# Kernel optimization log

Hardware: AMD Instinct MI355X
Metric: run time of the kernel (lower is better)

The kernel has to match this reference:

```python
import jax, jax.numpy as jnp
import numpy as np

N = 100000   # nodes
E = 1600000  # edges (avg degree 16)
F_IN, H1, H2, H3, C = 500, 200, 100, 40, 3


def setup_inputs() -> dict:
    key = jax.random.key(0)
    ks = jax.random.split(key, 10)
    def w(k, shape, fan_in):
        return jax.random.normal(k, shape, dtype=jnp.float32) / np.sqrt(fan_in)
    return {
        "x": jax.random.normal(ks[0], (N, F_IN), dtype=jnp.float32),
        "edge_index": jax.random.randint(ks[1], (2, E), 0, N, dtype=jnp.int32),
        "W1": w(ks[2], (H1, F_IN), F_IN), "b1": jnp.zeros((H1,), jnp.float32),
        "W1b": w(ks[3], (H2, H1), H1),  "b1b": jnp.zeros((H2,), jnp.float32),
        "W2b": w(ks[4], (H3, H2), H2),  "b2b": jnp.zeros((H3,), jnp.float32),
        "W2": w(ks[5], (C, H3), H3),    "b2": jnp.zeros((C,), jnp.float32),
    }


def _gcn_conv(x, W, b, src, dst, norm_e, n):
    # GCNConv: linear transform, then normalized scatter-add aggregation, then bias
    h = x @ W.T                                   # [N, out]
    msgs = h[src] * norm_e[:, None]               # [E+N, out] gathered, normalized
    out = jax.ops.segment_sum(msgs, dst, num_segments=n)
    return out + b


def reference(x, edge_index, W1, b1, W1b, b1b, W2b, b2b, W2, b2):
    n = x.shape[0]
    loop = jnp.arange(n, dtype=edge_index.dtype)
    src = jnp.concatenate([edge_index[0], loop])  # add self-loops (GCNConv default)
    dst = jnp.concatenate([edge_index[1], loop])
    # symmetric normalization: deg computed on target nodes, norm = d^-1/2[src]*d^-1/2[dst]
    deg = jax.ops.segment_sum(jnp.ones_like(dst, dtype=x.dtype), dst, num_segments=n)
    dinv = jnp.where(deg > 0, jax.lax.rsqrt(deg), 0.0)
    norm_e = dinv[src] * dinv[dst]

    # dropout(p=0.5, training=self.training) is identity at inference
    h = jax.nn.relu(_gcn_conv(x, W1, b1, src, dst, norm_e, n))
    h = jax.nn.relu(_gcn_conv(h, W1b, b1b, src, dst, norm_e, n))
    h = jax.nn.relu(_gcn_conv(h, W2b, b2b, src, dst, norm_e, n))
    return _gcn_conv(h, W2, b2, src, dst, norm_e, n)
```

## Files before the change

### kernel.cpp

```cpp
#include <hip/hip_runtime.h>


#define DEV __device__ __forceinline__

typedef __attribute__((ext_vector_type(8))) short short8;
typedef __attribute__((ext_vector_type(8))) _Float16 f16x8;
typedef __attribute__((ext_vector_type(4))) float f32x4;
typedef __attribute__((ext_vector_type(4))) _Float16 f16x4;

DEV unsigned short f2bf(float x) {
    unsigned u = __builtin_bit_cast(unsigned, x);
    u += 0x7FFFu + ((u >> 16) & 1u);
    return (unsigned short)(u >> 16);
}
DEV float bf2f(unsigned short b) {
    return __builtin_bit_cast(float, (unsigned)b << 16);
}

DEV void gload_lds16(const void* g, void* l) {
    __builtin_amdgcn_global_load_lds(
        (const __attribute__((address_space(1))) unsigned int*)g,
        (__attribute__((address_space(3))) unsigned int*)l, 16, 0, 0);
}


__global__ void k_init(int* __restrict__ cnt, int* __restrict__ fill, int n) {
    int i = blockIdx.x * 256 + threadIdx.x;
    if (i < n) { cnt[i] = 1; fill[i] = 0; }
}

__global__ void k_count(const int* __restrict__ dst, int* __restrict__ cnt, int E) {
    int e = blockIdx.x * 256 + threadIdx.x;
    if (e < E) atomicAdd(&cnt[dst[e]], 1);
}

__global__ void k_scan1(const int* __restrict__ cnt, int* __restrict__ row_start,
                        int* __restrict__ partial, float* __restrict__ dinv, int n) {
    __shared__ int sdata[256];
    int base = blockIdx.x * 1024;
    int t = threadIdx.x;
    int v[4]; int sum = 0;
#pragma unroll
    for (int j = 0; j < 4; ++j) {
        int idx = base + t * 4 + j;
        v[j] = (idx < n) ? cnt[idx] : 0;
        if (idx < n) dinv[idx] = rsqrtf((float)v[j]);
        sum += v[j];
    }
    sdata[t] = sum;
    __syncthreads();
    for (int off = 1; off < 256; off <<= 1) {
        int x = (t >= off) ? sdata[t - off] : 0;
        __syncthreads();
        sdata[t] += x;
        __syncthreads();
    }
    int excl = sdata[t] - sum;
#pragma unroll
    for (int j = 0; j < 4; ++j) {
        int idx = base + t * 4 + j;
        if (idx < n) row_start[idx] = excl;
        excl += v[j];
    }
    if (t == 255) partial[blockIdx.x] = sdata[255];
}

__global__ void k_scan2(int* __restrict__ partial, int nb) {
    __shared__ int s[128];
    int t = threadIdx.x;
    int v = (t < nb) ? partial[t] : 0;
    s[t] = v;
    __syncthreads();
    for (int off = 1; off < 128; off <<= 1) {
        int x = (t >= off) ? s[t - off] : 0;
        __syncthreads();
        s[t] += x;
        __syncthreads();
    }
    if (t < nb) partial[t] = s[t] - v;
}

__global__ void k_scan3(int* __restrict__ row_start, const int* __restrict__ partial,
                        int n, int total) {
    int i = blockIdx.x * 256 + threadIdx.x;
    if (i < n) row_start[i] += partial[i >> 10];
    if (i == 0) row_start[n] = total;
}

__global__ void k_fill(const int* __restrict__ src, const int* __restrict__ dst,
                       const int* __restrict__ row_start, int* __restrict__ fill,
                       int* __restrict__ csr_src, int E, int n) {
    int i = blockIdx.x * 256 + threadIdx.x;
    int total = E + n;
    if (i >= total) return;
    int s, d;
    if (i < E) { s = src[i]; d = dst[i]; }
    else       { s = d = i - E; }
    int pos = row_start[d] + atomicAdd(&fill[d], 1);
    csr_src[pos] = s;
}

__global__ void k_wdec(const float* __restrict__ W, int N, int K,
                       unsigned short* __restrict__ Wh, unsigned short* __restrict__ Wl,
                       int NPAD, int KPAD) {
    int i = blockIdx.x * 256 + threadIdx.x;
    if (i >= NPAD * KPAD) return;
    int r = i / KPAD, k = i - r * KPAD;
    float x = (r < N && k < K) ? W[r * K + k] : 0.f;
    unsigned short h = f2bf(x);
    unsigned short l = f2bf(x - bf2f(h));
    Wh[i] = h; Wl[i] = l;
}
__global__ void k_wdec16(const float* __restrict__ W, int N, int K,
                         unsigned short* __restrict__ Wh, unsigned short* __restrict__ Wl,
                         int NPAD, int KPAD) {
    int i = blockIdx.x * 256 + threadIdx.x;
    if (i >= NPAD * KPAD) return;
    int r = i / KPAD, k = i - r * KPAD;
    float x = (r < N && k < K) ? W[r * K + k] : 0.f;
    _Float16 h = (_Float16)x;
    _Float16 l = (_Float16)((x - (float)h) * 2048.0f);
    Wh[i] = __builtin_bit_cast(unsigned short, h);
    Wl[i] = __builtin_bit_cast(unsigned short, l);
}


struct A8 { f32x4 lo, hi; };

template <int NF, int MODE, typename AT>
__global__ __launch_bounds__(256, 2)
void gemm_mfma(const AT* __restrict__ A, int lda, int M, int K,
               const unsigned short* __restrict__ Wh,
               const unsigned short* __restrict__ Wl, int ldw,
               const float* __restrict__ dinv,
               _Float16* __restrict__ H16, int ldh, int Nout) {
    constexpr int NPAD = NF * 16;
    constexpr int HBUF = NPAD * 64;
    constexpr int BUFB = 2 * HBUF;
    constexpr int CH   = NPAD * 4;
    constexpr int CH2  = 2 * CH;
    constexpr int NISS = CH2 / 64;
    __shared__ char lds[2 * BUFB];

    const int tid  = threadIdx.x;
    const int wv   = tid >> 6;
    const int lane = tid & 63;
    const int lr   = lane & 15;
    const int kq   = lane >> 4;
    const int m0   = blockIdx.x * 128;

    int arow0 = m0 + wv * 32 + lr;       if (arow0 >= M) arow0 = M - 1;
    int arow1 = m0 + wv * 32 + 16 + lr;  if (arow1 >= M) arow1 = M - 1;
    const AT* Arow0 = A + (size_t)arow0 * lda;
    const AT* Arow1 = A + (size_t)arow1 * lda;

    auto stageW = [&](int s, int bufsel) {
        const int kb = s * 32;
        char* base = lds + bufsel * BUFB;
        for (int i = wv; i < NISS; i += 4) {
            int c  = i * 64 + lane;
            int h  = (c >= CH) ? 1 : 0;
            int cc = c - h * CH;
            int r  = cc >> 2;
            int sl = cc & 3;
            int gs = sl ^ (r & 3);
            const unsigned short* gp = (h ? Wl : Wh) + (size_t)r * ldw + kb + gs * 8;
            gload_lds16(gp, base + i * 1024);
        }
    };

    auto loadA32 = [&](const AT* Arow, int s) -> A8 {
        A8 o;
        int kb = s * 32 + kq * 8;
        if (kb + 8 <= K) {
            const float* ap = (const float*)Arow + kb;
            o.lo = *(const f32x4*)ap;
            o.hi = *(const f32x4*)(ap + 4);
        } else {
#pragma unroll
            for (int i = 0; i < 4; ++i) {
                int k0 = kb + i, k1 = kb + 4 + i;
                o.lo[i] = (k0 < K) ? (float)Arow[k0] : 0.f;
                o.hi[i] = (k1 < K) ? (float)Arow[k1] : 0.f;
            }
        }
        return o;
    };
    auto loadA16 = [&](const AT* Arow, int s) -> short8 {
        int kb = s * 32 + kq * 8;
        if (kb + 8 <= K) return *(const short8*)((const unsigned short*)Arow + kb);
        short8 o;
        const unsigned short* ap = (const unsigned short*)Arow;
#pragma unroll
        for (int i = 0; i < 8; ++i) o[i] = (kb + i < K) ? (short)ap[kb + i] : (short)0;
        return o;
    };

    f32x4 acP[NF], acQ[NF], alP[NF], alQ[NF];
#pragma unroll
    for (int f = 0; f < NF; ++f) {
        acP[f] = (f32x4){0.f, 0.f, 0.f, 0.f};
        acQ[f] = (f32x4){0.f, 0.f, 0.f, 0.f};
        alP[f] = (f32x4){0.f, 0.f, 0.f, 0.f};
        alQ[f] = (f32x4){0.f, 0.f, 0.f, 0.f};
    }

    const int nsteps = ldw / 32;

    stageW(0, 0);
    A8 a0c{}, a1c{}; short8 h0c{}, h1c{};
    if constexpr (MODE == 0) { a0c = loadA32(Arow0, 0); a1c = loadA32(Arow1, 0); }
    else                     { h0c = loadA16(Arow0, 0); h1c = loadA16(Arow1, 0); }
    __syncthreads();

    const int ro = lr * 64 + ((kq ^ (lr & 3)) << 4);

    for (int s = 0; s < nsteps; ++s) {
        const char* bb = lds + (s & 1) * BUFB;
        const bool more = (s + 1 < nsteps);

        if (more) stageW(s + 1, (s + 1) & 1);
        A8 a0n{}, a1n{}; short8 h0n{}, h1n{};
        if (more) {
            if constexpr (MODE == 0) { a0n = loadA32(Arow0, s + 1); a1n = loadA32(Arow1, s + 1); }
            else                     { h0n = loadA16(Arow0, s + 1); h1n = loadA16(Arow1, s + 1); }
        }

        if constexpr (MODE == 0) {
            float av0[8], av1[8];
#pragma unroll
            for (int i = 0; i < 4; ++i) {
                av0[i] = a0c.lo[i]; av0[4 + i] = a0c.hi[i];
                av1[i] = a1c.lo[i]; av1[4 + i] = a1c.hi[i];
            }
            short8 a0hi, a0lo, a1hi, a1lo;
#pragma unroll
            for (int i = 0; i < 8; ++i) {
                unsigned short h0 = f2bf(av0[i]);
                a0hi[i] = (short)h0; a0lo[i] = (short)f2bf(av0[i] - bf2f(h0));
                unsigned short h1 = f2bf(av1[i]);
                a1hi[i] = (short)h1; a1lo[i] = (short)f2bf(av1[i] - bf2f(h1));
            }
#pragma unroll
            for (int f = 0; f < NF; ++f) {
                short8 bh = *(const short8*)(bb + f * 1024 + ro);
                short8 bl = *(const short8*)(bb + HBUF + f * 1024 + ro);
                acP[f] = __builtin_amdgcn_mfma_f32_16x16x32_bf16(a0hi, bh, acP[f], 0, 0, 0);
                acP[f] = __builtin_amdgcn_mfma_f32_16x16x32_bf16(a0hi, bl, acP[f], 0, 0, 0);
                acP[f] = __builtin_amdgcn_mfma_f32_16x16x32_bf16(a0lo, bh, acP[f], 0, 0, 0);
                acQ[f] = __builtin_amdgcn_mfma_f32_16x16x32_bf16(a1hi, bh, acQ[f], 0, 0, 0);
                acQ[f] = __builtin_amdgcn_mfma_f32_16x16x32_bf16(a1hi, bl, acQ[f], 0, 0, 0);
                acQ[f] = __builtin_amdgcn_mfma_f32_16x16x32_bf16(a1lo, bh, acQ[f], 0, 0, 0);
            }
        } else {
            f16x8 a0 = __builtin_bit_cast(f16x8, h0c);
            f16x8 a1 = __builtin_bit_cast(f16x8, h1c);
#pragma unroll
            for (int f = 0; f < NF; ++f) {
                f16x8 bh = __builtin_bit_cast(f16x8, *(const short8*)(bb + f * 1024 + ro));
                f16x8 bl = __builtin_bit_cast(f16x8, *(const short8*)(bb + HBUF + f * 1024 + ro));
                acP[f] = __builtin_amdgcn_mfma_f32_16x16x32_f16(a0, bh, acP[f], 0, 0, 0);
                alP[f] = __builtin_amdgcn_mfma_f32_16x16x32_f16(a0, bl, alP[f], 0, 0, 0);
                acQ[f] = __builtin_amdgcn_mfma_f32_16x16x32_f16(a1, bh, acQ[f], 0, 0, 0);
                alQ[f] = __builtin_amdgcn_mfma_f32_16x16x32_f16(a1, bl, alQ[f], 0, 0, 0);
            }
        }

        __syncthreads();
        if constexpr (MODE == 0) { a0c = a0n; a1c = a1n; }
        else                     { h0c = h0n; h1c = h1n; }
    }

    {
        const int rbase = m0 + wv * 32 + kq * 4;
        float dv[4];
#pragma unroll
        for (int j = 0; j < 4; ++j) {
            int row = rbase + j;
            dv[j] = (row < M) ? dinv[row] : 0.f;
        }
#pragma unroll
        for (int f = 0; f < NF; ++f) {
            int col = f * 16 + lr;
            if (col >= Nout) continue;
#pragma unroll
            for (int j = 0; j < 4; ++j) {
                int row = rbase + j;
                if (row >= M) continue;
                float v = acP[f][j];
                if constexpr (MODE == 1) v += alP[f][j] * (1.0f / 2048.0f);
                H16[(size_t)row * ldh + col] = (_Float16)(v * dv[j]);
            }
        }
    }
    {
        const int rbase = m0 + wv * 32 + 16 + kq * 4;
        float dv[4];
#pragma unroll
        for (int j = 0; j < 4; ++j) {
            int row = rbase + j;
            dv[j] = (row < M) ? dinv[row] : 0.f;
        }
#pragma unroll
        for (int f = 0; f < NF; ++f) {
            int col = f * 16 + lr;
            if (col >= Nout) continue;
#pragma unroll
            for (int j = 0; j < 4; ++j) {
                int row = rbase + j;
                if (row >= M) continue;
                float v = acQ[f][j];
                if constexpr (MODE == 1) v += alQ[f][j] * (1.0f / 2048.0f);
                H16[(size_t)row * ldh + col] = (_Float16)(v * dv[j]);
            }
        }
    }
}


template <int F, bool RELU>
__global__ __launch_bounds__(256)
void agg_f16(const _Float16* __restrict__ h, const int* __restrict__ row_start,
             const int* __restrict__ csr_src, const float* __restrict__ dinv,
             const float* __restrict__ bias, _Float16* __restrict__ out, int n,
             int ldo) {
    constexpr int LPN = F / 4;
    constexpr int NPW = 64 / LPN;
    int wave = blockIdx.x * 4 + (threadIdx.x >> 6);
    int lane = threadIdx.x & 63;
    int sub  = lane / LPN;
    int fi   = lane - sub * LPN;
    int node = wave * NPW + sub;
    if (sub >= NPW || node >= n) return;
    int f = fi * 4;
    const _Float16* hf = h + f;

    f32x4 acc = {0.f, 0.f, 0.f, 0.f};
    int e0 = row_start[node], e1 = row_start[node + 1];
    int e = e0;
    for (; e + 4 <= e1; e += 4) {
        int s0 = csr_src[e + 0];
        int s1 = csr_src[e + 1];
        int s2 = csr_src[e + 2];
        int s3 = csr_src[e + 3];
        f16x4 v0 = *(const f16x4*)&hf[(size_t)s0 * F];
        f16x4 v1 = *(const f16x4*)&hf[(size_t)s1 * F];
        f16x4 v2 = *(const f16x4*)&hf[(size_t)s2 * F];
        f16x4 v3 = *(const f16x4*)&hf[(size_t)s3 * F];
        acc += __builtin_convertvector(v0, f32x4);
        acc += __builtin_convertvector(v1, f32x4);
        acc += __builtin_convertvector(v2, f32x4);
        acc += __builtin_convertvector(v3, f32x4);
    }
    for (; e < e1; ++e) {
        int s = csr_src[e];
        f16x4 v = *(const f16x4*)&hf[(size_t)s * F];
        acc += __builtin_convertvector(v, f32x4);
    }
    float dn = dinv[node];
    f32x4 b4 = *(const f32x4*)&bias[f];
    acc = acc * dn + b4;
    if (RELU) {
#pragma unroll
        for (int j = 0; j < 4; ++j) acc[j] = fmaxf(acc[j], 0.f);
    }
    f16x4 o;
#pragma unroll
    for (int j = 0; j < 4; ++j) o[j] = (_Float16)acc[j];
    *(f16x4*)&out[(size_t)node * ldo + f] = o;
}


__global__ void gemm_small(const _Float16* __restrict__ A, const float* __restrict__ B,
                           const float* __restrict__ dinv, float* __restrict__ C,
                           int M, int K) {
    int m = blockIdx.x * 256 + threadIdx.x;
    if (m >= M) return;
    float a0 = 0.f, a1 = 0.f, a2 = 0.f;
    for (int k = 0; k < K; ++k) {
        float a = (float)A[(size_t)m * K + k];
        a0 += a * B[0 * K + k];
        a1 += a * B[1 * K + k];
        a2 += a * B[2 * K + k];
    }
    float dv = dinv[m];
    C[(size_t)m * 3 + 0] = a0 * dv;
    C[(size_t)m * 3 + 1] = a1 * dv;
    C[(size_t)m * 3 + 2] = a2 * dv;
}

__global__ void agg_f3(const float* __restrict__ h, const int* __restrict__ row_start,
                       const int* __restrict__ csr_src, const float* __restrict__ dinv,
                       const float* __restrict__ bias, float* __restrict__ out, int n) {
    int i = blockIdx.x * 256 + threadIdx.x;
    if (i >= n * 3) return;
    int node = i / 3;
    int f = i - node * 3;
    float acc = 0.f;
    int e1 = row_start[node + 1];
    for (int e = row_start[node]; e < e1; ++e) {
        int s = csr_src[e];
        acc += h[(size_t)s * 3 + f];
    }
    out[i] = acc * dinv[node] + bias[f];
}


extern "C" void kernel_launch(void* const* d_in, const int* in_sizes, int n_in,
                              void* d_out, int out_size, void* d_ws, size_t ws_size,
                              hipStream_t stream) {
    const float* x   = (const float*)d_in[0];
    const int*   ei  = (const int*)d_in[1];
    const float* W1  = (const float*)d_in[2];
    const float* b1  = (const float*)d_in[3];
    const float* W1b = (const float*)d_in[4];
    const float* b1b = (const float*)d_in[5];
    const float* W2b = (const float*)d_in[6];
    const float* b2b = (const float*)d_in[7];
    const float* W2  = (const float*)d_in[8];
    const float* b2  = (const float*)d_in[9];
    float* out = (float*)d_out;

    const int F_IN = 500, H1 = 200, H2 = 100, H3 = 40;
    const int N = in_sizes[0] / F_IN;
    const int E = in_sizes[1] / 2;
    const int* src = ei;
    const int* dst = ei + E;

    size_t off = 0;
    auto alloc = [&](size_t bytes) -> void* {
        void* p = (char*)d_ws + off;
        off += (bytes + 255) & ~(size_t)255;
        return p;
    };
    int*   cnt       = (int*)  alloc((size_t)N * 4);
    int*   row_start = (int*)  alloc((size_t)(N + 1) * 4);
    int*   fill      = (int*)  alloc((size_t)N * 4);
    int*   partial   = (int*)  alloc(128 * 4);
    float* dinv      = (float*)alloc((size_t)N * 4);
    int*   csr_src   = (int*)  alloc((size_t)(E + N) * 4);
    unsigned short* wh1 = (unsigned short*)alloc(208 * 512 * 2);
    unsigned short* wl1 = (unsigned short*)alloc(208 * 512 * 2);
    unsigned short* wh2 = (unsigned short*)alloc(112 * 224 * 2);
    unsigned short* wl2 = (unsigned short*)alloc(112 * 224 * 2);
    unsigned short* wh3 = (unsigned short*)alloc(48 * 128 * 2);
    unsigned short* wl3 = (unsigned short*)alloc(48 * 128 * 2);
    _Float16* h16   = (_Float16*)alloc((size_t)N * H1 * 2);
    _Float16* act16 = (_Float16*)alloc((size_t)N * H1 * 2);
    float*    bufC  = (float*)   alloc((size_t)N * 3 * 4);

    int gN  = (N + 255) / 256;
    int gE  = (E + 255) / 256;
    int gEN = (E + N + 255) / 256;
    int nb  = (N + 1023) / 1024;

    k_init <<<gN, 256, 0, stream>>>(cnt, fill, N);
    k_count<<<gE, 256, 0, stream>>>(dst, cnt, E);
    k_scan1<<<nb, 256, 0, stream>>>(cnt, row_start, partial, dinv, N);
    k_scan2<<<1, 128, 0, stream>>>(partial, nb);
    k_scan3<<<gN, 256, 0, stream>>>(row_start, partial, N, E + N);
    k_fill <<<gEN, 256, 0, stream>>>(src, dst, row_start, fill, csr_src, E, N);

    k_wdec  <<<(208 * 512 + 255) / 256, 256, 0, stream>>>(W1,  H1, F_IN, wh1, wl1, 208, 512);
    k_wdec16<<<(112 * 224 + 255) / 256, 256, 0, stream>>>(W1b, H2, H1,   wh2, wl2, 112, 224);
    k_wdec16<<<( 48 * 128 + 255) / 256, 256, 0, stream>>>(W2b, H3, H2,   wh3, wl3,  48, 128);

    const int gG = (N + 127) / 128;

    gemm_mfma<13, 0, float><<<gG, 256, 0, stream>>>(x, F_IN, N, F_IN, wh1, wl1, 512,
                                                    dinv, h16, H1, H1);
    agg_f16<200, true><<<(N + 3) / 4, 256, 0, stream>>>(h16, row_start, csr_src, dinv,
                                                        b1, act16, N, 200);
    gemm_mfma<7, 1, _Float16><<<gG, 256, 0, stream>>>(act16, 200, N, H1, wh2, wl2, 224,
                                                      dinv, h16, H2, H2);
    agg_f16<100, true><<<(N / 2 + 3) / 4, 256, 0, stream>>>(h16, row_start, csr_src, dinv,
                                                            b1b, act16, N, 112);
    gemm_mfma<3, 1, _Float16><<<gG, 256, 0, stream>>>(act16, 112, N, H2, wh3, wl3, 128,
                                                      dinv, h16, H3, H3);
    {
        int waves = (N + 5) / 6, blocks = (waves + 3) / 4;
        agg_f16<40, true><<<blocks, 256, 0, stream>>>(h16, row_start, csr_src, dinv,
                                                      b2b, act16, N, 40);
    }
    gemm_small<<<(N + 255) / 256, 256, 0, stream>>>(act16, W2, dinv, bufC, N, H3);
    agg_f3<<<(N * 3 + 255) / 256, 256, 0, stream>>>(bufC, row_start, csr_src, dinv,
                                                    b2, out, N);
}
```

Measured before the change: 577.3 us.

## Load GEMM weights directly from global memory instead of LDS double-buffering

Removes the LDS staging of weight tiles, the double buffer and the per-step barriers from the MFMA GEMM. Each lane now reads its weight fragments straight from global memory, relying on L1/L2 caching of the small weight matrices. Blocks grow to 512 threads covering 256 rows, and the K dimension becomes a compile-time template parameter. The A-operand prefetch is also dropped, so load latency is exposed unless occupancy hides it, and weight reads are now redundant across waves.

```diff
diff --git a/kernel.cpp b/kernel.cpp
--- a/kernel.cpp
+++ b/kernel.cpp
@@ -15,12 +15,6 @@
 }
 DEV float bf2f(unsigned short b) {
     return __builtin_bit_cast(float, (unsigned)b << 16);
-}
-
-DEV void gload_lds16(const void* g, void* l) {
-    __builtin_amdgcn_global_load_lds(
-        (const __attribute__((address_space(1))) unsigned int*)g,
-        (__attribute__((address_space(3))) unsigned int*)l, 16, 0, 0);
 }
 
 
@@ -127,47 +121,27 @@
 
 struct A8 { f32x4 lo, hi; };
 
-template <int NF, int MODE, typename AT>
-__global__ __launch_bounds__(256, 2)
+template <int NF, int LDW, int MODE, typename AT>
+__global__ __launch_bounds__(512, 2)
 void gemm_mfma(const AT* __restrict__ A, int lda, int M, int K,
                const unsigned short* __restrict__ Wh,
-               const unsigned short* __restrict__ Wl, int ldw,
+               const unsigned short* __restrict__ Wl,
                const float* __restrict__ dinv,
                _Float16* __restrict__ H16, int ldh, int Nout) {
-    constexpr int NPAD = NF * 16;
-    constexpr int HBUF = NPAD * 64;
-    constexpr int BUFB = 2 * HBUF;
-    constexpr int CH   = NPAD * 4;
-    constexpr int CH2  = 2 * CH;
-    constexpr int NISS = CH2 / 64;
-    __shared__ char lds[2 * BUFB];
-
     const int tid  = threadIdx.x;
     const int wv   = tid >> 6;
     const int lane = tid & 63;
     const int lr   = lane & 15;
     const int kq   = lane >> 4;
-    const int m0   = blockIdx.x * 128;
+    const int m0   = blockIdx.x * 256;
 
     int arow0 = m0 + wv * 32 + lr;       if (arow0 >= M) arow0 = M - 1;
     int arow1 = m0 + wv * 32 + 16 + lr;  if (arow1 >= M) arow1 = M - 1;
     const AT* Arow0 = A + (size_t)arow0 * lda;
     const AT* Arow1 = A + (size_t)arow1 * lda;
 
-    auto stageW = [&](int s, int bufsel) {
-        const int kb = s * 32;
-        char* base = lds + bufsel * BUFB;
-        for (int i = wv; i < NISS; i += 4) {
-            int c  = i * 64 + lane;
-            int h  = (c >= CH) ? 1 : 0;
-            int cc = c - h * CH;
-            int r  = cc >> 2;
-            int sl = cc & 3;
-            int gs = sl ^ (r & 3);
-            const unsigned short* gp = (h ? Wl : Wh) + (size_t)r * ldw + kb + gs * 8;
-            gload_lds16(gp, base + i * 1024);
-        }
-    };
+    const unsigned short* WhL = Wh + (size_t)lr * LDW + kq * 8;
+    const unsigned short* WlL = Wl + (size_t)lr * LDW + kq * 8;
 
     auto loadA32 = [&](const AT* Arow, int s) -> A8 {
         A8 o;
@@ -205,33 +179,20 @@
         alQ[f] = (f32x4){0.f, 0.f, 0.f, 0.f};
     }
 
-    const int nsteps = ldw / 32;
-
-    stageW(0, 0);
-    A8 a0c{}, a1c{}; short8 h0c{}, h1c{};
-    if constexpr (MODE == 0) { a0c = loadA32(Arow0, 0); a1c = loadA32(Arow1, 0); }
-    else                     { h0c = loadA16(Arow0, 0); h1c = loadA16(Arow1, 0); }
-    __syncthreads();
-
-    const int ro = lr * 64 + ((kq ^ (lr & 3)) << 4);
+    constexpr int nsteps = LDW / 32;
 
     for (int s = 0; s < nsteps; ++s) {
-        const char* bb = lds + (s & 1) * BUFB;
-        const bool more = (s + 1 < nsteps);
-
-        if (more) stageW(s + 1, (s + 1) & 1);
-        A8 a0n{}, a1n{}; short8 h0n{}, h1n{};
-        if (more) {
-            if constexpr (MODE == 0) { a0n = loadA32(Arow0, s + 1); a1n = loadA32(Arow1, s + 1); }
-            else                     { h0n = loadA16(Arow0, s + 1); h1n = loadA16(Arow1, s + 1); }
-        }
+        const unsigned short* wph = WhL + s * 32;
+        const unsigned short* wpl = WlL + s * 32;
 
         if constexpr (MODE == 0) {
+            A8 a0 = loadA32(Arow0, s);
+            A8 a1 = loadA32(Arow1, s);
             float av0[8], av1[8];
 #pragma unroll
             for (int i = 0; i < 4; ++i) {
-                av0[i] = a0c.lo[i]; av0[4 + i] = a0c.hi[i];
-                av1[i] = a1c.lo[i]; av1[4 + i] = a1c.hi[i];
+                av0[i] = a0.lo[i]; av0[4 + i] = a0.hi[i];
+                av1[i] = a1.lo[i]; av1[4 + i] = a1.hi[i];
             }
             short8 a0hi, a0lo, a1hi, a1lo;
 #pragma unroll
@@ -243,8 +204,8 @@
             }
 #pragma unroll
             for (int f = 0; f < NF; ++f) {
-                short8 bh = *(const short8*)(bb + f * 1024 + ro);
-                short8 bl = *(const short8*)(bb + HBUF + f * 1024 + ro);
+                short8 bh = *(const short8*)(wph + (size_t)f * 16 * LDW);
+                short8 bl = *(const short8*)(wpl + (size_t)f * 16 * LDW);
                 acP[f] = __builtin_amdgcn_mfma_f32_16x16x32_bf16(a0hi, bh, acP[f], 0, 0, 0);
                 acP[f] = __builtin_amdgcn_mfma_f32_16x16x32_bf16(a0hi, bl, acP[f], 0, 0, 0);
                 acP[f] = __builtin_amdgcn_mfma_f32_16x16x32_bf16(a0lo, bh, acP[f], 0, 0, 0);
@@ -253,22 +214,18 @@
                 acQ[f] = __builtin_amdgcn_mfma_f32_16x16x32_bf16(a1lo, bh, acQ[f], 0, 0, 0);
             }
         } else {
-            f16x8 a0 = __builtin_bit_cast(f16x8, h0c);
-            f16x8 a1 = __builtin_bit_cast(f16x8, h1c);
+            f16x8 a0 = __builtin_bit_cast(f16x8, loadA16(Arow0, s));
+            f16x8 a1 = __builtin_bit_cast(f16x8, loadA16(Arow1, s));
 #pragma unroll
             for (int f = 0; f < NF; ++f) {
-                f16x8 bh = __builtin_bit_cast(f16x8, *(const short8*)(bb + f * 1024 + ro));
-                f16x8 bl = __builtin_bit_cast(f16x8, *(const short8*)(bb + HBUF + f * 1024 + ro));
+                f16x8 bh = __builtin_bit_cast(f16x8, *(const short8*)(wph + (size_t)f * 16 * LDW));
+                f16x8 bl = __builtin_bit_cast(f16x8, *(const short8*)(wpl + (size_t)f * 16 * LDW));
                 acP[f] = __builtin_amdgcn_mfma_f32_16x16x32_f16(a0, bh, acP[f], 0, 0, 0);
                 alP[f] = __builtin_amdgcn_mfma_f32_16x16x32_f16(a0, bl, alP[f], 0, 0, 0);
                 acQ[f] = __builtin_amdgcn_mfma_f32_16x16x32_f16(a1, bh, acQ[f], 0, 0, 0);
                 alQ[f] = __builtin_amdgcn_mfma_f32_16x16x32_f16(a1, bl, alQ[f], 0, 0, 0);
             }
         }
-
-        __syncthreads();
-        if constexpr (MODE == 0) { a0c = a0n; a1c = a1n; }
-        else                     { h0c = h0n; h1c = h1n; }
     }
 
     {
@@ -465,18 +422,18 @@
     k_wdec16<<<(112 * 224 + 255) / 256, 256, 0, stream>>>(W1b, H2, H1,   wh2, wl2, 112, 224);
     k_wdec16<<<( 48 * 128 + 255) / 256, 256, 0, stream>>>(W2b, H3, H2,   wh3, wl3,  48, 128);
 
-    const int gG = (N + 127) / 128;
-
-    gemm_mfma<13, 0, float><<<gG, 256, 0, stream>>>(x, F_IN, N, F_IN, wh1, wl1, 512,
-                                                    dinv, h16, H1, H1);
+    const int gG = (N + 255) / 256;
+
+    gemm_mfma<13, 512, 0, float><<<gG, 512, 0, stream>>>(x, F_IN, N, F_IN, wh1, wl1,
+                                                         dinv, h16, H1, H1);
     agg_f16<200, true><<<(N + 3) / 4, 256, 0, stream>>>(h16, row_start, csr_src, dinv,
                                                         b1, act16, N, 200);
-    gemm_mfma<7, 1, _Float16><<<gG, 256, 0, stream>>>(act16, 200, N, H1, wh2, wl2, 224,
-                                                      dinv, h16, H2, H2);
+    gemm_mfma<7, 224, 1, _Float16><<<gG, 512, 0, stream>>>(act16, 200, N, H1, wh2, wl2,
+                                                           dinv, h16, H2, H2);
     agg_f16<100, true><<<(N / 2 + 3) / 4, 256, 0, stream>>>(h16, row_start, csr_src, dinv,
                                                             b1b, act16, N, 112);
-    gemm_mfma<3, 1, _Float16><<<gG, 256, 0, stream>>>(act16, 112, N, H2, wh3, wl3, 128,
-                                                      dinv, h16, H3, H3);
+    gemm_mfma<3, 128, 1, _Float16><<<gG, 512, 0, stream>>>(act16, 112, N, H2, wh3, wl3,
+                                                           dinv, h16, H3, H3);
     {
         int waves = (N + 5) / 6, blocks = (waves + 3) / 4;
         agg_f16<40, true><<<blocks, 256, 0, stream>>>(h16, row_start, csr_src, dinv,
```

After: 780.9 us. +35.3%, slower.

## Use fp16 split-weight MFMA for first layer and split columns across 8 waves

Applied to the files above, without the earlier changes.

The first GEMM no longer splits x into bf16 hi/lo parts with three bf16 MFMAs per tile. It now converts x to a single fp16 value and uses the fp16 hi/lo weight split already used by the other layers, so all layers share one code path. Each GEMM block grows to 512 threads, with wave pairs splitting the output column fragments, which halves accumulator registers per wave and adds parallelism. The risk is accuracy: x is rounded to fp16 and its low part is dropped, and fp16 has less exponent range than bf16.

```diff
diff --git a/kernel.cpp b/kernel.cpp
--- a/kernel.cpp
+++ b/kernel.cpp
@@ -7,15 +7,6 @@
 typedef __attribute__((ext_vector_type(8))) _Float16 f16x8;
 typedef __attribute__((ext_vector_type(4))) float f32x4;
 typedef __attribute__((ext_vector_type(4))) _Float16 f16x4;
-
-DEV unsigned short f2bf(float x) {
-    unsigned u = __builtin_bit_cast(unsigned, x);
-    u += 0x7FFFu + ((u >> 16) & 1u);
-    return (unsigned short)(u >> 16);
-}
-DEV float bf2f(unsigned short b) {
-    return __builtin_bit_cast(float, (unsigned)b << 16);
-}
 
 DEV void gload_lds16(const void* g, void* l) {
     __builtin_amdgcn_global_load_lds(
@@ -100,17 +91,7 @@
     csr_src[pos] = s;
 }
 
-__global__ void k_wdec(const float* __restrict__ W, int N, int K,
-                       unsigned short* __restrict__ Wh, unsigned short* __restrict__ Wl,
-                       int NPAD, int KPAD) {
-    int i = blockIdx.x * 256 + threadIdx.x;
-    if (i >= NPAD * KPAD) return;
-    int r = i / KPAD, k = i - r * KPAD;
-    float x = (r < N && k < K) ? W[r * K + k] : 0.f;
-    unsigned short h = f2bf(x);
-    unsigned short l = f2bf(x - bf2f(h));
-    Wh[i] = h; Wl[i] = l;
-}
+
 __global__ void k_wdec16(const float* __restrict__ W, int N, int K,
                          unsigned short* __restrict__ Wh, unsigned short* __restrict__ Wl,
                          int NPAD, int KPAD) {
@@ -128,7 +109,7 @@
 struct A8 { f32x4 lo, hi; };
 
 template <int NF, int MODE, typename AT>
-__global__ __launch_bounds__(256, 2)
+__global__ __launch_bounds__(512, 2)
 void gemm_mfma(const AT* __restrict__ A, int lda, int M, int K,
                const unsigned short* __restrict__ Wh,
                const unsigned short* __restrict__ Wl, int ldw,
@@ -140,24 +121,28 @@
     constexpr int CH   = NPAD * 4;
     constexpr int CH2  = 2 * CH;
     constexpr int NISS = CH2 / 64;
+    constexpr int FC   = (NF + 1) / 2;
     __shared__ char lds[2 * BUFB];
 
     const int tid  = threadIdx.x;
     const int wv   = tid >> 6;
+    const int rg   = wv >> 1;
+    const int cg   = wv & 1;
     const int lane = tid & 63;
     const int lr   = lane & 15;
     const int kq   = lane >> 4;
     const int m0   = blockIdx.x * 128;
-
-    int arow0 = m0 + wv * 32 + lr;       if (arow0 >= M) arow0 = M - 1;
-    int arow1 = m0 + wv * 32 + 16 + lr;  if (arow1 >= M) arow1 = M - 1;
+    const int f0   = cg * FC;
+
+    int arow0 = m0 + rg * 32 + lr;       if (arow0 >= M) arow0 = M - 1;
+    int arow1 = m0 + rg * 32 + 16 + lr;  if (arow1 >= M) arow1 = M - 1;
     const AT* Arow0 = A + (size_t)arow0 * lda;
     const AT* Arow1 = A + (size_t)arow1 * lda;
 
     auto stageW = [&](int s, int bufsel) {
         const int kb = s * 32;
         char* base = lds + bufsel * BUFB;
-        for (int i = wv; i < NISS; i += 4) {
+        for (int i = wv; i < NISS; i += 8) {
             int c  = i * 64 + lane;
             int h  = (c >= CH) ? 1 : 0;
             int cc = c - h * CH;
@@ -195,14 +180,23 @@
         for (int i = 0; i < 8; ++i) o[i] = (kb + i < K) ? (short)ap[kb + i] : (short)0;
         return o;
     };
-
-    f32x4 acP[NF], acQ[NF], alP[NF], alQ[NF];
-#pragma unroll
-    for (int f = 0; f < NF; ++f) {
-        acP[f] = (f32x4){0.f, 0.f, 0.f, 0.f};
-        acQ[f] = (f32x4){0.f, 0.f, 0.f, 0.f};
-        alP[f] = (f32x4){0.f, 0.f, 0.f, 0.f};
-        alQ[f] = (f32x4){0.f, 0.f, 0.f, 0.f};
+    auto cvtA = [&](const A8& a) -> f16x8 {
+        f16x8 o;
+#pragma unroll
+        for (int i = 0; i < 4; ++i) {
+            o[i]     = (_Float16)a.lo[i];
+            o[4 + i] = (_Float16)a.hi[i];
+        }
+        return o;
+    };
+
+    f32x4 acP[FC], alP[FC], acQ[FC], alQ[FC];
+#pragma unroll
+    for (int ff = 0; ff < FC; ++ff) {
+        acP[ff] = (f32x4){0.f, 0.f, 0.f, 0.f};
+        alP[ff] = (f32x4){0.f, 0.f, 0.f, 0.f};
+        acQ[ff] = (f32x4){0.f, 0.f, 0.f, 0.f};
+        alQ[ff] = (f32x4){0.f, 0.f, 0.f, 0.f};
     }
 
     const int nsteps = ldw / 32;
@@ -226,43 +220,20 @@
             else                     { h0n = loadA16(Arow0, s + 1); h1n = loadA16(Arow1, s + 1); }
         }
 
-        if constexpr (MODE == 0) {
-            float av0[8], av1[8];
-#pragma unroll
-            for (int i = 0; i < 4; ++i) {
-                av0[i] = a0c.lo[i]; av0[4 + i] = a0c.hi[i];
-                av1[i] = a1c.lo[i]; av1[4 + i] = a1c.hi[i];
-            }
-            short8 a0hi, a0lo, a1hi, a1lo;
-#pragma unroll
-            for (int i = 0; i < 8; ++i) {
-                unsigned short h0 = f2bf(av0[i]);
-                a0hi[i] = (short)h0; a0lo[i] = (short)f2bf(av0[i] - bf2f(h0));
-                unsigned short h1 = f2bf(av1[i]);
-                a1hi[i] = (short)h1; a1lo[i] = (short)f2bf(av1[i] - bf2f(h1));
-            }
-#pragma unroll
-            for (int f = 0; f < NF; ++f) {
-                short8 bh = *(const short8*)(bb + f * 1024 + ro);
-                short8 bl = *(const short8*)(bb + HBUF + f * 1024 + ro);
-                acP[f] = __builtin_amdgcn_mfma_f32_16x16x32_bf16(a0hi, bh, acP[f], 0, 0, 0);
-                acP[f] = __builtin_amdgcn_mfma_f32_16x16x32_bf16(a0hi, bl, acP[f], 0, 0, 0);
-                acP[f] = __builtin_amdgcn_mfma_f32_16x16x32_bf16(a0lo, bh, acP[f], 0, 0, 0);
-                acQ[f] = __builtin_amdgcn_mfma_f32_16x16x32_bf16(a1hi, bh, acQ[f], 0, 0, 0);
-                acQ[f] = __builtin_amdgcn_mfma_f32_16x16x32_bf16(a1hi, bl, acQ[f], 0, 0, 0);
-                acQ[f] = __builtin_amdgcn_mfma_f32_16x16x32_bf16(a1lo, bh, acQ[f], 0, 0, 0);
-            }
-        } else {
-            f16x8 a0 = __builtin_bit_cast(f16x8, h0c);
-            f16x8 a1 = __builtin_bit_cast(f16x8, h1c);
-#pragma unroll
-            for (int f = 0; f < NF; ++f) {
+        f16x8 a0, a1;
+        if constexpr (MODE == 0) { a0 = cvtA(a0c); a1 = cvtA(a1c); }
+        else { a0 = __builtin_bit_cast(f16x8, h0c); a1 = __builtin_bit_cast(f16x8, h1c); }
+
+#pragma unroll
+        for (int ff = 0; ff < FC; ++ff) {
+            int f = f0 + ff;
+            if (f < NF) {
                 f16x8 bh = __builtin_bit_cast(f16x8, *(const short8*)(bb + f * 1024 + ro));
                 f16x8 bl = __builtin_bit_cast(f16x8, *(const short8*)(bb + HBUF + f * 1024 + ro));
-                acP[f] = __builtin_amdgcn_mfma_f32_16x16x32_f16(a0, bh, acP[f], 0, 0, 0);
-                alP[f] = __builtin_amdgcn_mfma_f32_16x16x32_f16(a0, bl, alP[f], 0, 0, 0);
-                acQ[f] = __builtin_amdgcn_mfma_f32_16x16x32_f16(a1, bh, acQ[f], 0, 0, 0);
-                alQ[f] = __builtin_amdgcn_mfma_f32_16x16x32_f16(a1, bl, alQ[f], 0, 0, 0);
+                acP[ff] = __builtin_amdgcn_mfma_f32_16x16x32_f16(a0, bh, acP[ff], 0, 0, 0);
+                alP[ff] = __builtin_amdgcn_mfma_f32_16x16x32_f16(a0, bl, alP[ff], 0, 0, 0);
+                acQ[ff] = __builtin_amdgcn_mfma_f32_16x16x32_f16(a1, bh, acQ[ff], 0, 0, 0);
+                alQ[ff] = __builtin_amdgcn_mfma_f32_16x16x32_f16(a1, bl, alQ[ff], 0, 0, 0);
             }
         }
 
@@ -272,7 +243,7 @@
     }
 
     {
-        const int rbase = m0 + wv * 32 + kq * 4;
+        const int rbase = m0 + rg * 32 + kq * 4;
         float dv[4];
 #pragma unroll
         for (int j = 0; j < 4; ++j) {
@@ -280,21 +251,22 @@
             dv[j] = (row < M) ? dinv[row] : 0.f;
         }
 #pragma unroll
-        for (int f = 0; f < NF; ++f) {
+        for (int ff = 0; ff < FC; ++ff) {
+            int f = f0 + ff;
+            if (f >= NF) continue;
             int col = f * 16 + lr;
             if (col >= Nout) continue;
 #pragma unroll
             for (int j = 0; j < 4; ++j) {
                 int row = rbase + j;
                 if (row >= M) continue;
-                float v = acP[f][j];
-                if constexpr (MODE == 1) v += alP[f][j] * (1.0f / 2048.0f);
+                float v = acP[ff][j] + alP[ff][j] * (1.0f / 2048.0f);
                 H16[(size_t)row * ldh + col] = (_Float16)(v * dv[j]);
             }
         }
     }
     {
-        const int rbase = m0 + wv * 32 + 16 + kq * 4;
+        const int rbase = m0 + rg * 32 + 16 + kq * 4;
         float dv[4];
 #pragma unroll
         for (int j = 0; j < 4; ++j) {
@@ -302,15 +274,16 @@
             dv[j] = (row < M) ? dinv[row] : 0.f;
         }
 #pragma unroll
-        for (int f = 0; f < NF; ++f) {
+        for (int ff = 0; ff < FC; ++ff) {
+            int f = f0 + ff;
+            if (f >= NF) continue;
             int col = f * 16 + lr;
             if (col >= Nout) continue;
 #pragma unroll
             for (int j = 0; j < 4; ++j) {
                 int row = rbase + j;
                 if (row >= M) continue;
-                float v = acQ[f][j];
-                if constexpr (MODE == 1) v += alQ[f][j] * (1.0f / 2048.0f);
+                float v = acQ[ff][j] + alQ[ff][j] * (1.0f / 2048.0f);
                 H16[(size_t)row * ldh + col] = (_Float16)(v * dv[j]);
             }
         }
@@ -461,21 +434,21 @@
     k_scan3<<<gN, 256, 0, stream>>>(row_start, partial, N, E + N);
     k_fill <<<gEN, 256, 0, stream>>>(src, dst, row_start, fill, csr_src, E, N);
 
-    k_wdec  <<<(208 * 512 + 255) / 256, 256, 0, stream>>>(W1,  H1, F_IN, wh1, wl1, 208, 512);
+    k_wdec16<<<(208 * 512 + 255) / 256, 256, 0, stream>>>(W1,  H1, F_IN, wh1, wl1, 208, 512);
     k_wdec16<<<(112 * 224 + 255) / 256, 256, 0, stream>>>(W1b, H2, H1,   wh2, wl2, 112, 224);
     k_wdec16<<<( 48 * 128 + 255) / 256, 256, 0, stream>>>(W2b, H3, H2,   wh3, wl3,  48, 128);
 
     const int gG = (N + 127) / 128;
 
-    gemm_mfma<13, 0, float><<<gG, 256, 0, stream>>>(x, F_IN, N, F_IN, wh1, wl1, 512,
+    gemm_mfma<13, 0, float><<<gG, 512, 0, stream>>>(x, F_IN, N, F_IN, wh1, wl1, 512,
                                                     dinv, h16, H1, H1);
     agg_f16<200, true><<<(N + 3) / 4, 256, 0, stream>>>(h16, row_start, csr_src, dinv,
                                                         b1, act16, N, 200);
-    gemm_mfma<7, 1, _Float16><<<gG, 256, 0, stream>>>(act16, 200, N, H1, wh2, wl2, 224,
+    gemm_mfma<7, 1, _Float16><<<gG, 512, 0, stream>>>(act16, 200, N, H1, wh2, wl2, 224,
                                                       dinv, h16, H2, H2);
     agg_f16<100, true><<<(N / 2 + 3) / 4, 256, 0, stream>>>(h16, row_start, csr_src, dinv,
                                                             b1b, act16, N, 112);
-    gemm_mfma<3, 1, _Float16><<<gG, 256, 0, stream>>>(act16, 112, N, H2, wh3, wl3, 128,
+    gemm_mfma<3, 1, _Float16><<<gG, 512, 0, stream>>>(act16, 112, N, H2, wh3, wl3, 128,
                                                       dinv, h16, H3, H3);
     {
         int waves = (N + 5) / 6, blocks = (waves + 3) / 4;
```

Result: slower. 603.6 us (+4.6%).
